# Performance work log

Hardware: AMD Instinct MI355X
Metric: run time of the kernel (lower is better)

## Reference

```python
import jax, jax.numpy as jnp
import numpy as np

ROWS, COLS = 4096, 8192
K = 4096                      # target_mask_size (<= COLS)
TEMPERATURE = 2.0 / 3.0


def setup_inputs() -> dict:
    key = jax.random.key(0)
    k1, k2 = jax.random.split(key)
    # param_init_fn: normal(mean=log(1-0.5)-log(0.5)=0, std=0.01)
    z_loga = jax.random.normal(k1, (ROWS, COLS), dtype=jnp.float32) * 0.01
    # eps = rand_like(...).clamp_(1e-6, 1-1e-6)
    eps = jax.random.uniform(k2, (ROWS, COLS), dtype=jnp.float32,
                             minval=1e-6, maxval=1.0 - 1e-6)
    return {"z_loga": z_loga, "eps": eps, "step": 0}


def reference(z_loga, eps, step):
    # Training branch of Mask.sample_z: gumbel-sigmoid + per-row top-k hard mask
    # with straight-through estimator.
    gumbel = -jnp.log(-jnp.log(eps))                       # [R, C]
    gumbel_mask = jax.nn.sigmoid((z_loga + gumbel) / TEMPERATURE)
    # per-row top-k hard selection (dim=1), scatter ones at top-k indices
    _, idx = jax.lax.top_k(gumbel_mask, K)                 # [R, K]
    rows = jnp.arange(gumbel_mask.shape[0])[:, None]       # [R, 1]
    hard = jnp.zeros_like(gumbel_mask).at[rows, idx].set(1.0)
    # straight-through: forward = hard, gradient flows through gumbel_mask
    st = hard - jax.lax.stop_gradient(gumbel_mask) + gumbel_mask
    return st.reshape(ROWS, COLS)                          # mask_output_shape
```

## Files before the change

### kernel.cpp

```cpp
#include <hip/hip_runtime.h>
#include <math.h>
#include <stdint.h>

#define ROWS 4096
#define COLS 8192
#define KSEL 4096
#define NT 256
#define NBINS 1024
#define WMAX 128
#define RANGE_HI 0.75f
#define LN2F 0.69314718056f

__device__ __forceinline__ int bin_of(float u) {
    int b = (int)(u * ((float)NBINS / RANGE_HI));
    b = b < 0 ? 0 : b;
    b = b > NBINS - 1 ? NBINS - 1 : b;
    return b;
}

__global__ __launch_bounds__(NT) void mask_topk_kernel(
    const float* __restrict__ z, const float* __restrict__ eps,
    float* __restrict__ out)
{
    __shared__ float    keys[COLS];
    __shared__ uint32_t hist[NBINS];
    __shared__ uint32_t scanbuf[NT];
    __shared__ int      winIdx[WMAX];
    __shared__ uint32_t winSig[WMAX];
    __shared__ int      s_B, s_need2;
    __shared__ uint32_t s_SB, s_wcount;

    const int row = blockIdx.x;
    const int tid = threadIdx.x;
    const size_t rbase = (size_t)row * COLS;

    for (int i = tid; i < NBINS; i += NT) hist[i] = 0;
    if (tid == 0) s_wcount = 0;
    __syncthreads();

    const float4* z4 = (const float4*)(z + rbase);
    const float4* e4 = (const float4*)(eps + rbase);
    for (int k = tid; k < COLS / 4; k += NT) {
        float4 zv = z4[k], ev = e4[k];
        float zz[4] = {zv.x, zv.y, zv.z, zv.w};
        float ee[4] = {ev.x, ev.y, ev.z, ev.w};
        float uu[4];
#pragma unroll
        for (int i = 0; i < 4; ++i) {
            float l1 = __builtin_amdgcn_logf(ee[i]) * LN2F;
            float l2 = __builtin_amdgcn_logf(-l1) * LN2F;
            uu[i] = zz[i] - l2;
            atomicAdd(&hist[bin_of(uu[i])], 1u);
        }
        float4 uv; uv.x = uu[0]; uv.y = uu[1]; uv.z = uu[2]; uv.w = uu[3];
        ((float4*)keys)[k] = uv;
    }
    __syncthreads();

    const int hb = tid * (NBINS / NT);
    uint32_t cs = 0;
#pragma unroll
    for (int i = 0; i < NBINS / NT; ++i) cs += hist[hb + i];
    scanbuf[tid] = cs;
    __syncthreads();
    for (int off = 1; off < NT; off <<= 1) {
        uint32_t v = scanbuf[tid];
        uint32_t add = (tid + off < NT) ? scanbuf[tid + off] : 0u;
        __syncthreads();
        scanbuf[tid] = v + add;
        __syncthreads();
    }
    uint32_t cum = (tid + 1 < NT) ? scanbuf[tid + 1] : 0u;
    for (int b = hb + NBINS / NT - 1; b >= hb; --b) {
        uint32_t h = hist[b];
        if (cum < KSEL && KSEL <= cum + h) { s_B = b; s_SB = cum; }
        cum += h;
    }
    __syncthreads();
    const int B = s_B;
    if (tid == 0) {
        uint32_t A = s_SB - ((B + 1 < NBINS) ? hist[B + 1] : 0u);
        s_need2 = KSEL - (int)A;
    }
    __syncthreads();
    const int need2 = s_need2;

    float4* o4 = (float4*)(out + rbase);
    for (int k = tid; k < COLS / 4; k += NT) {
        float4 uv = ((const float4*)keys)[k];
        float uu[4] = {uv.x, uv.y, uv.z, uv.w};
        float oo[4];
#pragma unroll
        for (int i = 0; i < 4; ++i) {
            int b = bin_of(uu[i]);
            oo[i] = (b > B + 1) ? 1.0f : 0.0f;
            if (b >= B - 1 && b <= B + 1) {
                uint32_t slot = atomicAdd(&s_wcount, 1u);
                if (slot < WMAX) winIdx[slot] = k * 4 + i;
            }
        }
        float4 ov; ov.x = oo[0]; ov.y = oo[1]; ov.z = oo[2]; ov.w = oo[3];
        o4[k] = ov;
    }
    __syncthreads();

    int w = (int)s_wcount; if (w > WMAX) w = WMAX;
    if (tid < 64) {
        for (int j = tid; j < w; j += 64) {
            int idx = winIdx[j];
            float e  = eps[rbase + idx];
            float zz = z[rbase + idx];
            float l1  = (float)log((double)e);
            float l2  = (float)log((double)(-l1));
            float g   = -l2;
            float s   = zz + g;
            float t   = s / (2.0f / 3.0f);
            float ex  = (float)exp(-(double)t);
            float sig = 1.0f / (1.0f + ex);
            winSig[j] = __float_as_uint(sig);
        }
    }
    __syncthreads();
    if (tid < 64) {
        for (int j = tid; j < w; j += 64) {
            uint32_t sj = winSig[j];
            int ij = winIdx[j];
            int rank = 0;
            for (int kk = 0; kk < w; ++kk) {
                uint32_t sk = winSig[kk];
                int ik = winIdx[kk];
                rank += (sk > sj || (sk == sj && ik < ij)) ? 1 : 0;
            }
            out[rbase + ij] = (rank < need2) ? 1.0f : 0.0f;
        }
    }
}

extern "C" void kernel_launch(void* const* d_in, const int* in_sizes, int n_in,
                              void* d_out, int out_size, void* d_ws, size_t ws_size,
                              hipStream_t stream) {
    const float* z   = (const float*)d_in[0];
    const float* eps = (const float*)d_in[1];
    float* out = (float*)d_out;
    hipLaunchKernelGGL(mask_topk_kernel, dim3(ROWS), dim3(NT), 0, stream,
                       z, eps, out);
}
```

Baseline: 324.2 us.

## Keep keys in registers, per-wave histograms, and wave-shuffle scan

Drops the 32KB shared-memory keys buffer and holds each thread's 32 keys in registers, which cuts LDS use and lets more blocks share a CU (launch bounds now request 5). The histogram is split into one copy per wave to reduce atomic contention, and the block-wide LDS scan, which had a barrier on every step, is replaced by wave shuffles plus a small per-wave total. The cost is higher register pressure and an extra reduction across the per-wave histograms.

```diff
diff --git a/kernel.cpp b/kernel.cpp
--- a/kernel.cpp
+++ b/kernel.cpp
@@ -6,6 +6,8 @@
 #define COLS 8192
 #define KSEL 4096
 #define NT 256
+#define NWAVE (NT / 64)
+#define PT (COLS / (4 * NT))
 #define NBINS 1024
 #define WMAX 128
 #define RANGE_HI 0.75f
@@ -18,85 +20,100 @@
     return b;
 }
 
-__global__ __launch_bounds__(NT) void mask_topk_kernel(
+__global__ __launch_bounds__(NT, 5) void mask_topk_kernel(
     const float* __restrict__ z, const float* __restrict__ eps,
     float* __restrict__ out)
 {
-    __shared__ float    keys[COLS];
-    __shared__ uint32_t hist[NBINS];
-    __shared__ uint32_t scanbuf[NT];
+    __shared__ uint32_t hist[NWAVE][NBINS];
+    __shared__ uint32_t wtot[NWAVE];
     __shared__ int      winIdx[WMAX];
     __shared__ uint32_t winSig[WMAX];
     __shared__ int      s_B, s_need2;
     __shared__ uint32_t s_SB, s_wcount;
 
-    const int row = blockIdx.x;
-    const int tid = threadIdx.x;
+    const int row  = blockIdx.x;
+    const int tid  = threadIdx.x;
+    const int lane = tid & 63;
+    const int wave = tid >> 6;
     const size_t rbase = (size_t)row * COLS;
 
-    for (int i = tid; i < NBINS; i += NT) hist[i] = 0;
+    for (int i = tid; i < NWAVE * NBINS; i += NT) ((uint32_t*)hist)[i] = 0;
     if (tid == 0) s_wcount = 0;
     __syncthreads();
 
     const float4* z4 = (const float4*)(z + rbase);
     const float4* e4 = (const float4*)(eps + rbase);
-    for (int k = tid; k < COLS / 4; k += NT) {
+    float u[4 * PT];
+#pragma unroll
+    for (int it = 0; it < PT; ++it) {
+        const int k = it * NT + tid;
         float4 zv = z4[k], ev = e4[k];
         float zz[4] = {zv.x, zv.y, zv.z, zv.w};
         float ee[4] = {ev.x, ev.y, ev.z, ev.w};
-        float uu[4];
 #pragma unroll
-        for (int i = 0; i < 4; ++i) {
-            float l1 = __builtin_amdgcn_logf(ee[i]) * LN2F;
+        for (int j = 0; j < 4; ++j) {
+            float l1 = __builtin_amdgcn_logf(ee[j]) * LN2F;
             float l2 = __builtin_amdgcn_logf(-l1) * LN2F;
-            uu[i] = zz[i] - l2;
-            atomicAdd(&hist[bin_of(uu[i])], 1u);
+            float uu = zz[j] - l2;
+            u[it * 4 + j] = uu;
+            atomicAdd(&hist[wave][bin_of(uu)], 1u);
         }
-        float4 uv; uv.x = uu[0]; uv.y = uu[1]; uv.z = uu[2]; uv.w = uu[3];
-        ((float4*)keys)[k] = uv;
     }
     __syncthreads();
 
     const int hb = tid * (NBINS / NT);
+    uint32_t h[NBINS / NT];
     uint32_t cs = 0;
 #pragma unroll
-    for (int i = 0; i < NBINS / NT; ++i) cs += hist[hb + i];
-    scanbuf[tid] = cs;
+    for (int i = 0; i < NBINS / NT; ++i) {
+        uint32_t t = 0;
+#pragma unroll
+        for (int c = 0; c < NWAVE; ++c) t += hist[c][hb + i];
+        h[i] = t;
+        cs += t;
+    }
+    uint32_t v = cs;
+#pragma unroll
+    for (int off = 1; off < 64; off <<= 1) {
+        uint32_t t = __shfl_down(v, off, 64);
+        if (lane + off < 64) v += t;
+    }
+    if (lane == 0) wtot[wave] = v;
     __syncthreads();
-    for (int off = 1; off < NT; off <<= 1) {
-        uint32_t v = scanbuf[tid];
-        uint32_t add = (tid + off < NT) ? scanbuf[tid + off] : 0u;
-        __syncthreads();
-        scanbuf[tid] = v + add;
-        __syncthreads();
-    }
-    uint32_t cum = (tid + 1 < NT) ? scanbuf[tid + 1] : 0u;
-    for (int b = hb + NBINS / NT - 1; b >= hb; --b) {
-        uint32_t h = hist[b];
-        if (cum < KSEL && KSEL <= cum + h) { s_B = b; s_SB = cum; }
-        cum += h;
+    uint32_t above = 0;
+#pragma unroll
+    for (int c = 0; c < NWAVE; ++c) above += (c > wave) ? wtot[c] : 0u;
+    uint32_t S_incl = v + above;
+    uint32_t cum = S_incl - cs;
+
+    for (int i = NBINS / NT - 1; i >= 0; --i) {
+        if (cum < KSEL && KSEL <= cum + h[i]) { s_B = hb + i; s_SB = cum; }
+        cum += h[i];
     }
     __syncthreads();
     const int B = s_B;
     if (tid == 0) {
-        uint32_t A = s_SB - ((B + 1 < NBINS) ? hist[B + 1] : 0u);
+        uint32_t hB1 = 0;
+        if (B + 1 < NBINS)
+            for (int c = 0; c < NWAVE; ++c) hB1 += hist[c][B + 1];
+        uint32_t A = s_SB - hB1;
         s_need2 = KSEL - (int)A;
     }
     __syncthreads();
     const int need2 = s_need2;
 
     float4* o4 = (float4*)(out + rbase);
-    for (int k = tid; k < COLS / 4; k += NT) {
-        float4 uv = ((const float4*)keys)[k];
-        float uu[4] = {uv.x, uv.y, uv.z, uv.w};
+#pragma unroll
+    for (int it = 0; it < PT; ++it) {
+        const int k = it * NT + tid;
         float oo[4];
 #pragma unroll
-        for (int i = 0; i < 4; ++i) {
-            int b = bin_of(uu[i]);
-            oo[i] = (b > B + 1) ? 1.0f : 0.0f;
+        for (int j = 0; j < 4; ++j) {
+            int b = bin_of(u[it * 4 + j]);
+            oo[j] = (b > B + 1) ? 1.0f : 0.0f;
             if (b >= B - 1 && b <= B + 1) {
                 uint32_t slot = atomicAdd(&s_wcount, 1u);
-                if (slot < WMAX) winIdx[slot] = k * 4 + i;
+                if (slot < WMAX) winIdx[slot] = k * 4 + j;
             }
         }
         float4 ov; ov.x = oo[0]; ov.y = oo[1]; ov.z = oo[2]; ov.w = oo[3];
@@ -106,7 +123,7 @@
 
     int w = (int)s_wcount; if (w > WMAX) w = WMAX;
     if (tid < 64) {
-        for (int j = tid; j < w; j += 64) {
+        for (int j = lane; j < w; j += 64) {
             int idx = winIdx[j];
             float e  = eps[rbase + idx];
             float zz = z[rbase + idx];
@@ -122,7 +139,7 @@
     }
     __syncthreads();
     if (tid < 64) {
-        for (int j = tid; j < w; j += 64) {
+        for (int j = lane; j < w; j += 64) {
             uint32_t sj = winSig[j];
             int ij = winIdx[j];
             int rank = 0;
```

Result: no change. 322.1 us (-0.6%).
